# Kernel optimization log

Hardware: AMD Instinct MI355X
Metric: run time of the kernel (lower is better)

Reference implementation:

```python
import jax, jax.numpy as jnp
import numpy as np


def setup_inputs() -> dict:
    key = jax.random.key(0)
    kq, kk, kv = jax.random.split(key, 3)
    B, H, L, D = 1, 16, 4096, 64
    q = jax.random.normal(kq, (B, H, L, D), dtype=jnp.float32)
    k = jax.random.normal(kk, (B, H, L, D), dtype=jnp.float32)
    v = jax.random.normal(kv, (B, H, L, D), dtype=jnp.float32)
    return {"q": q, "k": k, "v": v}


def reference(q, k, v):
    # scale = sqrt(head_dim), matching q.size(-1) ** 0.5 in the torch module
    scale = jnp.asarray(q.shape[-1], q.dtype) ** 0.5
    # [b,h,l,m] attention scores, materialized as in the original (no flash tiling)
    attn = jnp.einsum('bhlk,bhmk->bhlm', q, k) / scale
    attn = jax.nn.softmax(attn, axis=-1)
    out = jnp.einsum('bhlm,bhmk->bhlk', attn, v)
    return out
```

## Files before the change

kernel.cpp:

```cpp
#include <hip/hip_runtime.h>
#include <hip/hip_bf16.h>


#define LSEQ 4096
#define DH   64
#define NH   16
#define QBLK 128
#define KBLK 64
#define NT   (LSEQ / KBLK)

typedef float  f32x4   __attribute__((ext_vector_type(4)));
typedef short  short8v __attribute__((ext_vector_type(8)));

__device__ __forceinline__ short f2bf(float f) {
    unsigned int u = __builtin_bit_cast(unsigned int, f);
    u = (u + 0x7FFFu + ((u >> 16) & 1u)) >> 16;
    return (short)u;
}

__device__ __forceinline__ short8v pack8(const float4& a, const float4& b) {
    short8v f;
    f[0] = f2bf(a.x); f[1] = f2bf(a.y); f[2] = f2bf(a.z); f[3] = f2bf(a.w);
    f[4] = f2bf(b.x); f[5] = f2bf(b.y); f[6] = f2bf(b.z); f[7] = f2bf(b.w);
    return f;
}

#define SWZ(row, slot) ((((slot) ^ ((row) & 7)) << 3))

template <int NSPLIT>
__global__ __launch_bounds__(256, 2)
void attn_fwd(const float* __restrict__ q, const float* __restrict__ k,
              const float* __restrict__ v, float* __restrict__ out,
              float* __restrict__ opart, float* __restrict__ lpart) {
    __shared__ __align__(16) short Klds[KBLK][64];
    __shared__ __align__(16) short Vtlds[DH][64];
    __shared__ __align__(16) short Plds[4][32][64];

    const int t    = threadIdx.x;
    const int w    = t >> 6;
    const int lane = t & 63;
    const int g    = lane >> 4;
    const int c    = lane & 15;
    const int h     = blockIdx.y;
    const int qtile = blockIdx.x;
    const int z     = blockIdx.z;
    constexpr int nts = NT / NSPLIT;
    const int kt0   = z * nts;

    const float* qg = q + ((size_t)h * LSEQ + (size_t)qtile * QBLK) * DH;
    const float* kg = k + (size_t)h * LSEQ * DH;
    const float* vg = v + (size_t)h * LSEQ * DH;

    const int krow0 = t >> 3;
    const int kslot = t & 7;
    const int vd    = t & 63;
    const int vhalf = t >> 6;

    short8v qf[2][2];
    #pragma unroll
    for (int f = 0; f < 2; ++f) {
        const int qrow = w * 32 + f * 16 + c;
        #pragma unroll
        for (int h2 = 0; h2 < 2; ++h2) {
            const float* p = &qg[(size_t)qrow * DH + h2 * 32 + g * 8];
            float4 a = *(const float4*)p;
            float4 b = *(const float4*)(p + 4);
            short8v fr;
            fr[0] = f2bf(a.x * 0.125f); fr[1] = f2bf(a.y * 0.125f);
            fr[2] = f2bf(a.z * 0.125f); fr[3] = f2bf(a.w * 0.125f);
            fr[4] = f2bf(b.x * 0.125f); fr[5] = f2bf(b.y * 0.125f);
            fr[6] = f2bf(b.z * 0.125f); fr[7] = f2bf(b.w * 0.125f);
            qf[f][h2] = fr;
        }
    }

    f32x4 o[2][4];
    #pragma unroll
    for (int f = 0; f < 2; ++f)
        #pragma unroll
        for (int i = 0; i < 4; ++i) o[f][i] = (f32x4){0.f, 0.f, 0.f, 0.f};
    float lp[2][4] = {{0.f,0.f,0.f,0.f},{0.f,0.f,0.f,0.f}};

    float4 kreg[4];
    float  vreg[16];

    {
        const int keyP = kt0 * KBLK;
        #pragma unroll
        for (int i = 0; i < 2; ++i) {
            const float* p = &kg[(size_t)(keyP + krow0 + i * 32) * DH + kslot * 8];
            kreg[2*i]   = *(const float4*)p;
            kreg[2*i+1] = *(const float4*)(p + 4);
        }
        #pragma unroll
        for (int j = 0; j < 16; ++j)
            vreg[j] = vg[(size_t)(keyP + vhalf * 16 + j) * DH + vd];
        const int ksw = krow0 & 7;
        #pragma unroll
        for (int i = 0; i < 2; ++i)
            *(short8v*)&Klds[krow0 + i*32][(kslot ^ ksw) << 3] = pack8(kreg[2*i], kreg[2*i+1]);
        #pragma unroll
        for (int i = 0; i < 2; ++i) {
            short8v f8;
            #pragma unroll
            for (int j = 0; j < 8; ++j) f8[j] = f2bf(vreg[i*8 + j]);
            *(short8v*)&Vtlds[vd][SWZ(vd, vhalf*2 + i)] = f8;
        }
    }
    __syncthreads();

    short* Pw = &Plds[w][0][0];

    for (int kt = kt0; kt < kt0 + nts; ++kt) {
        if (kt + 1 < kt0 + nts) {
            const int key1 = (kt + 1) * KBLK;
            #pragma unroll
            for (int i = 0; i < 2; ++i) {
                const float* p = &kg[(size_t)(key1 + krow0 + i * 32) * DH + kslot * 8];
                kreg[2*i]   = *(const float4*)p;
                kreg[2*i+1] = *(const float4*)(p + 4);
            }
            #pragma unroll
            for (int j = 0; j < 16; ++j)
                vreg[j] = vg[(size_t)(key1 + vhalf * 16 + j) * DH + vd];
        }

        f32x4 sf[2][4];
        #pragma unroll
        for (int kb = 0; kb < 4; ++kb) {
            const int krow = kb * 16 + c;
            const int sw   = c & 7;
            short8v k0 = *(const short8v*)&Klds[krow][(g       ^ sw) << 3];
            short8v k1 = *(const short8v*)&Klds[krow][((4 + g) ^ sw) << 3];
            #pragma unroll
            for (int f = 0; f < 2; ++f) {
                f32x4 acc = (f32x4){0.f, 0.f, 0.f, 0.f};
                acc = __builtin_amdgcn_mfma_f32_16x16x32_bf16(qf[f][0], k0, acc, 0, 0, 0);
                acc = __builtin_amdgcn_mfma_f32_16x16x32_bf16(qf[f][1], k1, acc, 0, 0, 0);
                sf[f][kb] = acc;
            }
        }

        #pragma unroll
        for (int f = 0; f < 2; ++f) {
            #pragma unroll
            for (int kb = 0; kb < 4; ++kb) {
                #pragma unroll
                for (int r = 0; r < 4; ++r) {
                    float pv = __expf(sf[f][kb][r]);
                    lp[f][r] += pv;
                    const int row = f * 16 + 4 * g + r;
                    const int col = kb * 16 + c;
                    Pw[row * 64 + SWZ(row, col >> 3) + (col & 7)] = f2bf(pv);
                }
            }
        }

        #pragma unroll
        for (int kt2 = 0; kt2 < 2; ++kt2) {
            const int slot = kt2 * 4 + g;
            short8v pa0 = *(const short8v*)&Pw[(c)      * 64 + SWZ(c, slot)];
            short8v pa1 = *(const short8v*)&Pw[(16 + c) * 64 + SWZ(16 + c, slot)];
            #pragma unroll
            for (int nf = 0; nf < 4; ++nf) {
                const int vrow = nf * 16 + c;
                short8v vb = *(const short8v*)&Vtlds[vrow][SWZ(vrow, slot)];
                o[0][nf] = __builtin_amdgcn_mfma_f32_16x16x32_bf16(pa0, vb, o[0][nf], 0, 0, 0);
                o[1][nf] = __builtin_amdgcn_mfma_f32_16x16x32_bf16(pa1, vb, o[1][nf], 0, 0, 0);
            }
        }

        if (kt + 1 < kt0 + nts) {
            __syncthreads();
            const int ksw = krow0 & 7;
            #pragma unroll
            for (int i = 0; i < 2; ++i)
                *(short8v*)&Klds[krow0 + i*32][(kslot ^ ksw) << 3] = pack8(kreg[2*i], kreg[2*i+1]);
            #pragma unroll
            for (int i = 0; i < 2; ++i) {
                short8v f8;
                #pragma unroll
                for (int j = 0; j < 8; ++j) f8[j] = f2bf(vreg[i*8 + j]);
                *(short8v*)&Vtlds[vd][SWZ(vd, vhalf*2 + i)] = f8;
            }
            __syncthreads();
        }
    }

    #pragma unroll
    for (int mask = 1; mask < 16; mask <<= 1) {
        #pragma unroll
        for (int f = 0; f < 2; ++f)
            #pragma unroll
            for (int r = 0; r < 4; ++r)
                lp[f][r] += __shfl_xor(lp[f][r], mask, 64);
    }

    if (NSPLIT == 1) {
        float* og = out + ((size_t)h * LSEQ + (size_t)qtile * QBLK) * DH;
        #pragma unroll
        for (int f = 0; f < 2; ++f)
            #pragma unroll
            for (int r = 0; r < 4; ++r) {
                float inv = 1.0f / lp[f][r];
                const int qrow = w * 32 + f * 16 + 4 * g + r;
                #pragma unroll
                for (int nf = 0; nf < 4; ++nf)
                    og[(size_t)qrow * DH + nf * 16 + c] = o[f][nf][r] * inv;
            }
    } else {
        float* op = opart + ((size_t)(z * NH + h) * LSEQ + (size_t)qtile * QBLK) * DH;
        float* lprow = lpart + (size_t)(z * NH + h) * LSEQ + (size_t)qtile * QBLK;
        #pragma unroll
        for (int f = 0; f < 2; ++f)
            #pragma unroll
            for (int r = 0; r < 4; ++r) {
                const int qrow = w * 32 + f * 16 + 4 * g + r;
                #pragma unroll
                for (int nf = 0; nf < 4; ++nf)
                    op[(size_t)qrow * DH + nf * 16 + c] = o[f][nf][r];
                if (c == 0) lprow[qrow] = lp[f][r];
            }
    }
}

__global__ __launch_bounds__(256)
void reduce_split(const float* __restrict__ opart, const float* __restrict__ lpart,
                  float* __restrict__ out) {
    const size_t OSZ  = (size_t)NH * LSEQ * DH;
    const size_t LSZ  = (size_t)NH * LSEQ;
    const size_t TOT4 = OSZ / 4;
    for (size_t i4 = (size_t)blockIdx.x * blockDim.x + threadIdx.x; i4 < TOT4;
         i4 += (size_t)gridDim.x * blockDim.x) {
        const size_t i   = i4 * 4;
        const size_t row = i >> 6;
        float4 a = *(const float4*)&opart[i];
        float4 b = *(const float4*)&opart[OSZ + i];
        float inv = 1.0f / (lpart[row] + lpart[LSZ + row]);
        float4 r;
        r.x = (a.x + b.x) * inv; r.y = (a.y + b.y) * inv;
        r.z = (a.z + b.z) * inv; r.w = (a.w + b.w) * inv;
        *(float4*)&out[i] = r;
    }
}

extern "C" void kernel_launch(void* const* d_in, const int* in_sizes, int n_in,
                              void* d_out, int out_size, void* d_ws, size_t ws_size,
                              hipStream_t stream) {
    const float* q = (const float*)d_in[0];
    const float* k = (const float*)d_in[1];
    const float* v = (const float*)d_in[2];
    float* out = (float*)d_out;

    const size_t OSZ = (size_t)NH * LSEQ * DH;
    const size_t LSZ = (size_t)NH * LSEQ;
    const size_t need = (2 * OSZ + 2 * LSZ) * sizeof(float);

    if (ws_size >= need) {
        float* opart = (float*)d_ws;
        float* lpart = opart + 2 * OSZ;
        attn_fwd<2><<<dim3(LSEQ / QBLK, NH, 2), dim3(256), 0, stream>>>(q, k, v, out, opart, lpart);
        reduce_split<<<dim3(2048), dim3(256), 0, stream>>>(opart, lpart, out);
    } else {
        attn_fwd<1><<<dim3(LSEQ / QBLK, NH, 1), dim3(256), 0, stream>>>(q, k, v, out, nullptr, nullptr);
    }
}
```

Measured before the change: 231.3 us.

## Double-buffer K/V tiles in LDS with 512-thread blocks and MFMA priority

```diff
diff --git a/kernel.cpp b/kernel.cpp
--- a/kernel.cpp
+++ b/kernel.cpp
@@ -5,7 +5,7 @@
 #define LSEQ 4096
 #define DH   64
 #define NH   16
-#define QBLK 128
+#define QBLK 256
 #define KBLK 64
 #define NT   (LSEQ / KBLK)
 
@@ -28,13 +28,13 @@
 #define SWZ(row, slot) ((((slot) ^ ((row) & 7)) << 3))
 
 template <int NSPLIT>
-__global__ __launch_bounds__(256, 2)
+__global__ __launch_bounds__(512, 4)
 void attn_fwd(const float* __restrict__ q, const float* __restrict__ k,
               const float* __restrict__ v, float* __restrict__ out,
               float* __restrict__ opart, float* __restrict__ lpart) {
-    __shared__ __align__(16) short Klds[KBLK][64];
-    __shared__ __align__(16) short Vtlds[DH][64];
-    __shared__ __align__(16) short Plds[4][32][64];
+    __shared__ __align__(16) short Klds[2][KBLK][64];
+    __shared__ __align__(16) short Vtlds[2][DH][64];
+    __shared__ __align__(16) short Plds[8][32][64];
 
     const int t    = threadIdx.x;
     const int w    = t >> 6;
@@ -51,10 +51,10 @@
     const float* kg = k + (size_t)h * LSEQ * DH;
     const float* vg = v + (size_t)h * LSEQ * DH;
 
-    const int krow0 = t >> 3;
+    const int krow  = t >> 3;
     const int kslot = t & 7;
     const int vd    = t & 63;
-    const int vhalf = t >> 6;
+    const int vs    = t >> 6;
 
     short8v qf[2][2];
     #pragma unroll
@@ -81,57 +81,65 @@
         for (int i = 0; i < 4; ++i) o[f][i] = (f32x4){0.f, 0.f, 0.f, 0.f};
     float lp[2][4] = {{0.f,0.f,0.f,0.f},{0.f,0.f,0.f,0.f}};
 
-    float4 kreg[4];
-    float  vreg[16];
+    float4 kreg[2];
+    float  vreg[8];
 
     {
         const int keyP = kt0 * KBLK;
-        #pragma unroll
-        for (int i = 0; i < 2; ++i) {
-            const float* p = &kg[(size_t)(keyP + krow0 + i * 32) * DH + kslot * 8];
-            kreg[2*i]   = *(const float4*)p;
-            kreg[2*i+1] = *(const float4*)(p + 4);
-        }
-        #pragma unroll
-        for (int j = 0; j < 16; ++j)
-            vreg[j] = vg[(size_t)(keyP + vhalf * 16 + j) * DH + vd];
-        const int ksw = krow0 & 7;
-        #pragma unroll
-        for (int i = 0; i < 2; ++i)
-            *(short8v*)&Klds[krow0 + i*32][(kslot ^ ksw) << 3] = pack8(kreg[2*i], kreg[2*i+1]);
-        #pragma unroll
-        for (int i = 0; i < 2; ++i) {
+        const float* p = &kg[(size_t)(keyP + krow) * DH + kslot * 8];
+        kreg[0] = *(const float4*)p;
+        kreg[1] = *(const float4*)(p + 4);
+        #pragma unroll
+        for (int j = 0; j < 8; ++j)
+            vreg[j] = vg[(size_t)(keyP + vs * 8 + j) * DH + vd];
+        *(short8v*)&Klds[0][krow][SWZ(krow, kslot)] = pack8(kreg[0], kreg[1]);
+        short8v f8;
+        #pragma unroll
+        for (int j = 0; j < 8; ++j) f8[j] = f2bf(vreg[j]);
+        *(short8v*)&Vtlds[0][vd][SWZ(vd, vs)] = f8;
+    }
+    if (nts > 1) {
+        const int key1 = (kt0 + 1) * KBLK;
+        const float* p = &kg[(size_t)(key1 + krow) * DH + kslot * 8];
+        kreg[0] = *(const float4*)p;
+        kreg[1] = *(const float4*)(p + 4);
+        #pragma unroll
+        for (int j = 0; j < 8; ++j)
+            vreg[j] = vg[(size_t)(key1 + vs * 8 + j) * DH + vd];
+    }
+    __syncthreads();
+
+    short* Pw = &Plds[w][0][0];
+
+    for (int it = 0; it < nts; ++it) {
+        const int cur = it & 1;
+        const int nxt = cur ^ 1;
+
+        if (it + 1 < nts) {
+            *(short8v*)&Klds[nxt][krow][SWZ(krow, kslot)] = pack8(kreg[0], kreg[1]);
             short8v f8;
             #pragma unroll
-            for (int j = 0; j < 8; ++j) f8[j] = f2bf(vreg[i*8 + j]);
-            *(short8v*)&Vtlds[vd][SWZ(vd, vhalf*2 + i)] = f8;
-        }
-    }
-    __syncthreads();
-
-    short* Pw = &Plds[w][0][0];
-
-    for (int kt = kt0; kt < kt0 + nts; ++kt) {
-        if (kt + 1 < kt0 + nts) {
-            const int key1 = (kt + 1) * KBLK;
-            #pragma unroll
-            for (int i = 0; i < 2; ++i) {
-                const float* p = &kg[(size_t)(key1 + krow0 + i * 32) * DH + kslot * 8];
-                kreg[2*i]   = *(const float4*)p;
-                kreg[2*i+1] = *(const float4*)(p + 4);
-            }
-            #pragma unroll
-            for (int j = 0; j < 16; ++j)
-                vreg[j] = vg[(size_t)(key1 + vhalf * 16 + j) * DH + vd];
+            for (int j = 0; j < 8; ++j) f8[j] = f2bf(vreg[j]);
+            *(short8v*)&Vtlds[nxt][vd][SWZ(vd, vs)] = f8;
+        }
+        if (it + 2 < nts) {
+            const int key2 = (kt0 + it + 2) * KBLK;
+            const float* p = &kg[(size_t)(key2 + krow) * DH + kslot * 8];
+            kreg[0] = *(const float4*)p;
+            kreg[1] = *(const float4*)(p + 4);
+            #pragma unroll
+            for (int j = 0; j < 8; ++j)
+                vreg[j] = vg[(size_t)(key2 + vs * 8 + j) * DH + vd];
         }
 
         f32x4 sf[2][4];
         #pragma unroll
         for (int kb = 0; kb < 4; ++kb) {
-            const int krow = kb * 16 + c;
-            const int sw   = c & 7;
-            short8v k0 = *(const short8v*)&Klds[krow][(g       ^ sw) << 3];
-            short8v k1 = *(const short8v*)&Klds[krow][((4 + g) ^ sw) << 3];
+            const int kr = kb * 16 + c;
+            const int sw = c & 7;
+            short8v k0 = *(const short8v*)&Klds[cur][kr][(g       ^ sw) << 3];
+            short8v k1 = *(const short8v*)&Klds[cur][kr][((4 + g) ^ sw) << 3];
+            __builtin_amdgcn_s_setprio(1);
             #pragma unroll
             for (int f = 0; f < 2; ++f) {
                 f32x4 acc = (f32x4){0.f, 0.f, 0.f, 0.f};
@@ -139,6 +147,7 @@
                 acc = __builtin_amdgcn_mfma_f32_16x16x32_bf16(qf[f][1], k1, acc, 0, 0, 0);
                 sf[f][kb] = acc;
             }
+            __builtin_amdgcn_s_setprio(0);
         }
 
         #pragma unroll
@@ -161,30 +170,18 @@
             const int slot = kt2 * 4 + g;
             short8v pa0 = *(const short8v*)&Pw[(c)      * 64 + SWZ(c, slot)];
             short8v pa1 = *(const short8v*)&Pw[(16 + c) * 64 + SWZ(16 + c, slot)];
+            __builtin_amdgcn_s_setprio(1);
             #pragma unroll
             for (int nf = 0; nf < 4; ++nf) {
                 const int vrow = nf * 16 + c;
-                short8v vb = *(const short8v*)&Vtlds[vrow][SWZ(vrow, slot)];
+                short8v vb = *(const short8v*)&Vtlds[cur][vrow][SWZ(vrow, slot)];
                 o[0][nf] = __builtin_amdgcn_mfma_f32_16x16x32_bf16(pa0, vb, o[0][nf], 0, 0, 0);
                 o[1][nf] = __builtin_amdgcn_mfma_f32_16x16x32_bf16(pa1, vb, o[1][nf], 0, 0, 0);
             }
-        }
-
-        if (kt + 1 < kt0 + nts) {
-            __syncthreads();
-            const int ksw = krow0 & 7;
-            #pragma unroll
-            for (int i = 0; i < 2; ++i)
-                *(short8v*)&Klds[krow0 + i*32][(kslot ^ ksw) << 3] = pack8(kreg[2*i], kreg[2*i+1]);
-            #pragma unroll
-            for (int i = 0; i < 2; ++i) {
-                short8v f8;
-                #pragma unroll
-                for (int j = 0; j < 8; ++j) f8[j] = f2bf(vreg[i*8 + j]);
-                *(short8v*)&Vtlds[vd][SWZ(vd, vhalf*2 + i)] = f8;
-            }
-            __syncthreads();
-        }
+            __builtin_amdgcn_s_setprio(0);
+        }
+
+        __syncthreads();
     }
 
     #pragma unroll
@@ -259,9 +256,9 @@
     if (ws_size >= need) {
         float* opart = (float*)d_ws;
         float* lpart = opart + 2 * OSZ;
-        attn_fwd<2><<<dim3(LSEQ / QBLK, NH, 2), dim3(256), 0, stream>>>(q, k, v, out, opart, lpart);
+        attn_fwd<2><<<dim3(LSEQ / QBLK, NH, 2), dim3(512), 0, stream>>>(q, k, v, out, opart, lpart);
         reduce_split<<<dim3(2048), dim3(256), 0, stream>>>(opart, lpart, out);
     } else {
-        attn_fwd<1><<<dim3(LSEQ / QBLK, NH, 1), dim3(256), 0, stream>>>(q, k, v, out, nullptr, nullptr);
-    }
-}
+        attn_fwd<1><<<dim3(LSEQ / QBLK, NH, 1), dim3(512), 0, stream>>>(q, k, v, out, nullptr, nullptr);
+    }
+}
```

Result: slower. 382.2 us (+65.2%).
